# Kernel optimization log

Measured on AMD Instinct MI355X. Metric: run time of the kernel, lower is better.

Reference implementation:

```python
import jax, jax.numpy as jnp
import numpy as np

C = 1.0          # Poincare ball curvature
EPS = 1e-7       # clamp epsilon used by the torch code


def _expmap0(u, c=C):
    # geoopt PoincareBall.expmap0: tanh(sqrt(c)||u||) * u / (sqrt(c)||u||)
    sc = jnp.sqrt(c)
    n = jnp.maximum(jnp.linalg.norm(u, axis=-1, keepdims=True), 1e-15)
    return jnp.tanh(sc * n) * u / (sc * n)


def _hyp_dist_sq(x, y, c=C):
    # Pairwise squared Poincare distance WITHOUT materializing [nq,nc,d]:
    # d(x,y) = (2/sqrt(c)) * artanh(sqrt(c) * ||mobius_add(-x, y)||)
    # ||mobius_add(-x,y)||^2 expands into dot products and squared norms.
    dot = x @ y.T                                  # [nq, nc]
    xn = jnp.sum(x * x, axis=-1)[:, None]          # [nq, 1]
    yn = jnp.sum(y * y, axis=-1)[None, :]          # [1, nc]
    alpha = 1.0 - 2.0 * c * dot + c * yn
    beta = 1.0 - c * xn
    num_sq = alpha * alpha * xn - 2.0 * alpha * beta * dot + beta * beta * yn
    den = jnp.maximum(1.0 - 2.0 * c * dot + c * c * xn * yn, 1e-15)
    t = jnp.sqrt(c) * jnp.sqrt(jnp.maximum(num_sq, 0.0)) / den
    t = jnp.clip(t, 0.0, 1.0 - EPS)
    d = (2.0 / jnp.sqrt(c)) * jnp.arctanh(t)
    return d * d


def _project(x, We, be, Wh, bh, Ws, bs, scale_h):
    e = x @ We.T + be
    e = e / jnp.linalg.norm(e, axis=-1, keepdims=True)
    h = _expmap0((x @ Wh.T + bh) * scale_h)
    s = x @ Ws.T + bs
    s = s / jnp.linalg.norm(s, axis=-1, keepdims=True)
    return e, h, s


def setup_inputs() -> dict:
    key = jax.random.key(0)
    ks = jax.random.split(key, 12)
    D, NQ, NC = 768, 512, 65536
    def lin(k, out_d, in_d):
        lim = 1.0 / np.sqrt(in_d)
        k1, k2 = jax.random.split(k)
        W = jax.random.uniform(k1, (out_d, in_d), jnp.float32, -lim, lim)
        b = jax.random.uniform(k2, (out_d,), jnp.float32, -lim, lim)
        return W, b
    We, be = lin(ks[0], 32, D)
    Wh, bh = lin(ks[1], 16, D)
    Ws, bs = lin(ks[2], 16, D)
    W1, b1 = lin(ks[3], 32, D)
    W2, b2 = lin(ks[4], 3, 32)
    return {
        'x_q': jax.random.normal(ks[5], (NQ, D), jnp.float32),
        'x_c': jax.random.normal(ks[6], (NC, D), jnp.float32),
        'We': We, 'be': be, 'Wh': Wh, 'bh': bh, 'Ws': Ws, 'bs': bs,
        'scale_h': jnp.float32(0.3),
        'W1': W1, 'b1': b1, 'W2': W2, 'b2': b2,
    }


def reference(x_q, x_c, We, be, Wh, bh, Ws, bs, scale_h, W1, b1, W2, b2):
    # forward() projections for queries and corpus
    q_e, q_h, q_s = _project(x_q, We, be, Wh, bh, Ws, bs, scale_h)
    c_e, c_h, c_s = _project(x_c, We, be, Wh, bh, Ws, bs, scale_h)
    # get_weights(): softplus MLP on raw query embedding -> [nq, 3]
    w = jax.nn.softplus(jax.nn.relu(x_q @ W1.T + b1) @ W2.T + b2)
    # batch_retrieve math, fully vectorized
    dist_e = 2.0 - 2.0 * (q_e @ c_e.T)                       # unit vecs: ||a-b||^2
    dots = jnp.clip(q_s @ c_s.T, -1.0 + EPS, 1.0 - EPS)
    dist_s = jnp.arccos(dots) ** 2
    dist_h = _hyp_dist_sq(q_h, c_h)
    total = w[:, 0:1] * dist_e + w[:, 1:2] * dist_h + w[:, 2:3] * dist_s
    return -total
```

## Files before the change

kernel.cpp:

```cpp
#include <hip/hip_runtime.h>
#include <math.h>

#define NQ 512
#define NC 65536
#define DIM 768
#define PC_ROWS 128

typedef unsigned short u16;
typedef float f32x4 __attribute__((ext_vector_type(4)));
typedef short bf16x8 __attribute__((ext_vector_type(8)));

#define MFMA16(A, B, C) __builtin_amdgcn_mfma_f32_16x16x32_bf16(A, B, C, 0, 0, 0)

__device__ __forceinline__ u16 f2bf(float x) {
  union { float f; unsigned int u; } v; v.f = x;
  unsigned int r = v.u + 0x7fffu + ((v.u >> 16) & 1u);
  return (u16)(r >> 16);
}
__device__ __forceinline__ float bf2f(u16 h) {
  union { unsigned int u; float f; } v; v.u = ((unsigned int)h) << 16;
  return v.f;
}

__device__ __forceinline__ float acos_poly(float x) {
  float z = fabsf(x);
  float p = -0.0012624911f;
  p = fmaf(p, z, 0.0066700901f);
  p = fmaf(p, z, -0.0170881256f);
  p = fmaf(p, z, 0.0308918810f);
  p = fmaf(p, z, -0.0501743046f);
  p = fmaf(p, z, 0.0889789874f);
  p = fmaf(p, z, -0.2145988016f);
  p = fmaf(p, z, 1.5707963050f);
  float r = __builtin_amdgcn_sqrtf(1.0f - z) * p;
  return (x < 0.0f) ? (3.14159265358979f - r) : r;
}

__global__ __launch_bounds__(256) void transpose_w(
    const float* __restrict__ We, const float* __restrict__ Ws,
    const float* __restrict__ Wh, float* __restrict__ wt)
{
  int id = blockIdx.x * 256 + threadIdx.x;
  int k = id >> 6;
  int o = id & 63;
  float v = (o < 32) ? We[(size_t)o * DIM + k]
          : (o < 48) ? Ws[(size_t)(o - 32) * DIM + k]
                     : Wh[(size_t)(o - 48) * DIM + k];
  wt[id] = v;
}

__global__ __launch_bounds__(128) void proj_q(
    const float* __restrict__ xq,
    const float* __restrict__ We, const float* __restrict__ be,
    const float* __restrict__ Wh, const float* __restrict__ bh,
    const float* __restrict__ Ws, const float* __restrict__ bs,
    const float* __restrict__ shp,
    const float* __restrict__ W1, const float* __restrict__ b1,
    const float* __restrict__ W2, const float* __restrict__ b2,
    u16* __restrict__ qpak, float* __restrict__ qmeta)
{
  __shared__ __align__(16) float xrow[DIM];
  __shared__ float vals[96];
  __shared__ float reluv[32];
  __shared__ float hv[16];
  __shared__ float stats[8];
  const int t = threadIdx.x;
  const int q = blockIdx.x;

  for (int i = t; i < DIM; i += 128) xrow[i] = xq[(size_t)q * DIM + i];
  __syncthreads();

  if (t < 96) {
    const float* wr;
    float bias;
    if (t < 32)      { wr = We + (size_t)t * DIM;        bias = be[t]; }
    else if (t < 48) { wr = Ws + (size_t)(t - 32) * DIM; bias = bs[t - 32]; }
    else if (t < 64) { wr = Wh + (size_t)(t - 48) * DIM; bias = bh[t - 48]; }
    else             { wr = W1 + (size_t)(t - 64) * DIM; bias = b1[t - 64]; }
    const float4* x4 = (const float4*)xrow;
    const float4* w4 = (const float4*)wr;
    float acc = 0.0f;
    #pragma unroll 4
    for (int k = 0; k < DIM / 4; ++k) {
      float4 a = x4[k];
      float4 b = w4[k];
      acc = fmaf(a.x, b.x, acc);
      acc = fmaf(a.y, b.y, acc);
      acc = fmaf(a.z, b.z, acc);
      acc = fmaf(a.w, b.w, acc);
    }
    acc += bias;
    if (t >= 48 && t < 64) acc *= shp[0];
    vals[t] = acc;
  }
  __syncthreads();
  if (t < 32) reluv[t] = fmaxf(vals[64 + t], 0.0f);
  __syncthreads();

  if (t == 0) {
    float s = 0.0f;
    for (int j = 0; j < 32; ++j) s += vals[j] * vals[j];
    stats[0] = sqrtf(s);
  } else if (t == 1) {
    float s = 0.0f;
    for (int j = 32; j < 48; ++j) s += vals[j] * vals[j];
    stats[1] = sqrtf(s);
  } else if (t == 2) {
    float s = 0.0f;
    for (int j = 48; j < 64; ++j) s += vals[j] * vals[j];
    float n = fmaxf(sqrtf(s), 1e-15f);
    float f = tanhf(n) / n;
    float xn = 0.0f;
    for (int j = 0; j < 16; ++j) {
      float hj = vals[48 + j] * f;
      hv[j] = hj;
      xn += hj * hj;
    }
    stats[2] = xn;
    stats[3] = 1.0f - xn;
  } else if (t >= 3 && t < 6) {
    int m = t - 3;
    float s = 0.0f;
    for (int j = 0; j < 32; ++j) s = fmaf(reluv[j], W2[m * 32 + j], s);
    s += b2[m];
    stats[4 + m] = fmaxf(s, 0.0f) + log1pf(expf(-fabsf(s)));
  }
  __syncthreads();

  u16* qp = qpak + (size_t)q * 192;
  if (t < 32) {
    float v = vals[t] / stats[0];
    u16 hi = f2bf(v);
    u16 lo = f2bf(v - bf2f(hi));
    qp[t] = hi; qp[32 + t] = lo;
  } else if (t < 48) {
    int j = t - 32;
    float v = vals[t] / stats[1];
    u16 hi = f2bf(v);
    u16 lo = f2bf(v - bf2f(hi));
    qp[64 + j] = hi;  qp[80 + j] = hi;
    qp[96 + j] = lo;  qp[112 + j] = lo;
  } else if (t < 64) {
    int j = t - 48;
    float v = hv[j];
    u16 hi = f2bf(v);
    u16 lo = f2bf(v - bf2f(hi));
    qp[128 + j] = hi; qp[144 + j] = hi;
    qp[160 + j] = lo; qp[176 + j] = lo;
  } else if (t == 64) qmeta[(size_t)q * 8 + 0] = stats[2];
  else if (t == 65)   qmeta[(size_t)q * 8 + 1] = stats[3];
  else if (t >= 66 && t < 69) qmeta[(size_t)q * 8 + (t - 64)] = stats[4 + (t - 66)];
}

__global__ __launch_bounds__(512) void proj_corpus(
    const float* __restrict__ xc, const float* __restrict__ wt,
    const float* __restrict__ be, const float* __restrict__ bh,
    const float* __restrict__ bs, const float* __restrict__ shp,
    u16* __restrict__ cpak, float* __restrict__ cyn)
{
  __shared__ float lds[8320];
  float (*lxT)[132] = (float(*)[132])lds;
  float (*vals)[65] = (float(*)[65])lds;

  const int tid = threadIdx.x;
  const int lane = tid & 63;
  const int wv = __builtin_amdgcn_readfirstlane(tid >> 6);
  const int o0 = wv * 8;
  const int r0 = blockIdx.x * PC_ROWS;

  float acc0[8], acc1[8];
  #pragma unroll
  for (int j = 0; j < 8; ++j) { acc0[j] = 0.0f; acc1[j] = 0.0f; }

  for (int k0 = 0; k0 < DIM; k0 += 32) {
    __syncthreads();
    #pragma unroll
    for (int i = 0; i < 2; ++i) {
      int p = tid + 512 * i;
      int row = p >> 3;
      int kq = p & 7;
      const float4 v = *(const float4*)(xc + (size_t)(r0 + row) * DIM + k0 + 4 * kq);
      lxT[4 * kq + 0][row] = v.x;
      lxT[4 * kq + 1][row] = v.y;
      lxT[4 * kq + 2][row] = v.z;
      lxT[4 * kq + 3][row] = v.w;
    }
    __syncthreads();
    #pragma unroll
    for (int k = 0; k < 32; ++k) {
      const float xv0 = lxT[k][lane];
      const float xv1 = lxT[k][lane + 64];
      const float* wk = wt + (size_t)(k0 + k) * 64 + o0;
      #pragma unroll
      for (int j = 0; j < 8; ++j) {
        const float w = wk[j];
        acc0[j] = fmaf(xv0, w, acc0[j]);
        acc1[j] = fmaf(xv1, w, acc1[j]);
      }
    }
  }
  __syncthreads();

  const float sh = shp[0];
  #pragma unroll
  for (int j = 0; j < 8; ++j) {
    int o = o0 + j;
    float b = (o < 32) ? be[o] : (o < 48) ? bs[o - 32] : bh[o - 48];
    float v0 = acc0[j] + b;
    float v1 = acc1[j] + b;
    if (o >= 48) { v0 *= sh; v1 *= sh; }
    vals[lane][o] = v0;
    vals[lane + 64][o] = v1;
  }
  __syncthreads();

  const int part = tid >> 7;
  const int row = tid & 127;
  const size_t g = (size_t)(r0 + row);
  u16* cp = cpak + g * 128;
  if (part == 0) {
    float ssum = 0.0f;
    for (int j = 0; j < 32; ++j) ssum += vals[row][j] * vals[row][j];
    float inv = 1.0f / sqrtf(ssum);
    for (int j = 0; j < 32; ++j) {
      float v = vals[row][j] * inv;
      u16 hi = f2bf(v);
      cp[j] = hi;
      cp[32 + j] = f2bf(v - bf2f(hi));
    }
  } else if (part == 1) {
    float ssum = 0.0f;
    for (int j = 32; j < 48; ++j) ssum += vals[row][j] * vals[row][j];
    float inv = 1.0f / sqrtf(ssum);
    for (int j = 0; j < 16; ++j) {
      float v = vals[row][32 + j] * inv;
      u16 hi = f2bf(v);
      cp[64 + j] = hi;
      cp[80 + j] = f2bf(v - bf2f(hi));
    }
  } else if (part == 2) {
    float ssum = 0.0f;
    for (int j = 48; j < 64; ++j) ssum += vals[row][j] * vals[row][j];
    float n = fmaxf(sqrtf(ssum), 1e-15f);
    float f = tanhf(n) / n;
    float yn = 0.0f;
    for (int j = 0; j < 16; ++j) {
      float hj = vals[row][48 + j] * f;
      u16 hi = f2bf(hj);
      cp[96 + j] = hi;
      cp[112 + j] = f2bf(hj - bf2f(hi));
      yn += hj * hj;
    }
    cyn[g] = yn;
  }
}

#define CLIPC 0.99999988f

__device__ __forceinline__ float pair_score(
    float de, float dss, float dh,
    float xn, float beta, float w0, float w1, float w2, float yn)
{
  float dist_e = 2.0f - 2.0f * de;

  float dcl = fminf(fmaxf(dss, -CLIPC), CLIPC);
  float ac = acos_poly(dcl);
  float dist_s = ac * ac;

  float alpha = 1.0f - 2.0f * dh + yn;
  float ab = alpha * beta;
  float num = alpha * alpha * xn - 2.0f * ab * dh + beta * beta * yn;
  float den = fmaxf(1.0f - 2.0f * dh + xn * yn, 1e-15f);
  float t = __builtin_amdgcn_sqrtf(fmaxf(num, 0.0f)) * __builtin_amdgcn_rcpf(den);
  t = fminf(t, CLIPC);
  float dd = __logf((1.0f + t) * __builtin_amdgcn_rcpf(1.0f - t));
  float dist_h = dd * dd;

  return -(w0 * dist_e + w1 * dist_h + w2 * dist_s);
}

__global__ __launch_bounds__(256) void pairwise(
    const u16* __restrict__ cpak, const float* __restrict__ cyn,
    const u16* __restrict__ qpak, const float* __restrict__ qmeta,
    float* __restrict__ out)
{
  const int lane = threadIdx.x & 63;
  const int wv = threadIdx.x >> 6;
  const int lr = lane & 15;
  const int lg = lane >> 4;
  const int c0 = blockIdx.x * 128 + wv * 32;
  const int qbase = blockIdx.y * 256;

  bf16x8 Beh[2], Bel[2], Bsp[2], Bhp[2];
  float ynv[2];
  #pragma unroll
  for (int ct = 0; ct < 2; ++ct) {
    const u16* cb = cpak + (size_t)(c0 + ct * 16 + lr) * 128 + lg * 8;
    Beh[ct] = *(const bf16x8*)(cb + 0);
    Bel[ct] = *(const bf16x8*)(cb + 32);
    Bsp[ct] = *(const bf16x8*)(cb + 64);
    Bhp[ct] = *(const bf16x8*)(cb + 96);
    ynv[ct] = cyn[c0 + ct * 16 + lr];
  }

  #pragma unroll 1
  for (int qt = 0; qt < 16; ++qt) {
    const int q0 = qbase + qt * 16;
    const u16* qb = qpak + (size_t)(q0 + lr) * 192 + lg * 8;
    bf16x8 Aeh = *(const bf16x8*)(qb + 0);
    bf16x8 Ael = *(const bf16x8*)(qb + 32);
    bf16x8 Ash = *(const bf16x8*)(qb + 64);
    bf16x8 Asl = *(const bf16x8*)(qb + 96);
    bf16x8 Ahh = *(const bf16x8*)(qb + 128);
    bf16x8 Ahl = *(const bf16x8*)(qb + 160);

    float4 mv[4];
    float w2v[4];
    #pragma unroll
    for (int j = 0; j < 4; ++j) {
      const int q = q0 + lg * 4 + j;
      mv[j] = *(const float4*)(qmeta + (size_t)q * 8);
      w2v[j] = qmeta[(size_t)q * 8 + 4];
    }

    const f32x4 z = {0.0f, 0.0f, 0.0f, 0.0f};
    f32x4 aE[2], aS[2], aH[2];
    #pragma unroll
    for (int ct = 0; ct < 2; ++ct) {
      aE[ct] = MFMA16(Aeh, Beh[ct], z);
      aE[ct] = MFMA16(Ael, Beh[ct], aE[ct]);
      aE[ct] = MFMA16(Aeh, Bel[ct], aE[ct]);
      aS[ct] = MFMA16(Ash, Bsp[ct], z);
      aS[ct] = MFMA16(Asl, Bsp[ct], aS[ct]);
      aH[ct] = MFMA16(Ahh, Bhp[ct], z);
      aH[ct] = MFMA16(Ahl, Bhp[ct], aH[ct]);
    }

    #pragma unroll
    for (int j = 0; j < 4; ++j) {
      const int q = q0 + lg * 4 + j;
      #pragma unroll
      for (int ct = 0; ct < 2; ++ct) {
        float r = pair_score(aE[ct][j], aS[ct][j], aH[ct][j],
                             mv[j].x, mv[j].y, mv[j].z, mv[j].w, w2v[j],
                             ynv[ct]);
        out[(size_t)q * NC + c0 + ct * 16 + lr] = r;
      }
    }
  }
}

extern "C" void kernel_launch(void* const* d_in, const int* in_sizes, int n_in,
                              void* d_out, int out_size, void* d_ws, size_t ws_size,
                              hipStream_t stream) {
  const float* xq = (const float*)d_in[0];
  const float* xc = (const float*)d_in[1];
  const float* We = (const float*)d_in[2];
  const float* be = (const float*)d_in[3];
  const float* Wh = (const float*)d_in[4];
  const float* bh = (const float*)d_in[5];
  const float* Ws = (const float*)d_in[6];
  const float* bs = (const float*)d_in[7];
  const float* sh = (const float*)d_in[8];
  const float* W1 = (const float*)d_in[9];
  const float* b1 = (const float*)d_in[10];
  const float* W2 = (const float*)d_in[11];
  const float* b2 = (const float*)d_in[12];
  float* out = (float*)d_out;

  float* w = (float*)d_ws;
  u16* qpak = (u16*)w;
  float* qmeta = w + 49152;
  float* wt = qmeta + NQ * 8;
  u16* cpak = (u16*)(wt + DIM * 64);
  float* cyn = (wt + DIM * 64) + 4194304;

  transpose_w<<<DIM * 64 / 256, 256, 0, stream>>>(We, Ws, Wh, wt);
  proj_q<<<NQ, 128, 0, stream>>>(xq, We, be, Wh, bh, Ws, bs, sh, W1, b1, W2, b2,
                                 qpak, qmeta);
  proj_corpus<<<NC / PC_ROWS, 512, 0, stream>>>(xc, wt, be, bh, bs, sh, cpak, cyn);
  pairwise<<<dim3(NC / 128, 2, 1), 256, 0, stream>>>(cpak, cyn, qpak, qmeta, out);
}
```

Measured before the change: 476.0 us.

## Compute corpus projection with split-bf16 MFMA instead of scalar FMA

Replaces the scalar fp32 FMA loop in the corpus projection (65536x768 times 768x64) with bf16 MFMA 16x16x32. Each operand is split into hi and lo bf16 parts, and three products are accumulated to keep near-fp32 accuracy. Weights are pre-packed into the MFMA B-fragment layout by a new kernel. x tiles are converted to bf16 hi/lo and stored in LDS with an XOR swizzle. Block size drops to 256 threads, and the normalization epilogue is merged into two thread groups. The change targets the compute-bound FMA cost of the projection, which reads about 200 MB of x_c. It adds conversion work on the load path and slightly reduces precision.

```diff
diff --git a/kernel.cpp b/kernel.cpp
--- a/kernel.cpp
+++ b/kernel.cpp
@@ -20,6 +20,9 @@
 __device__ __forceinline__ float bf2f(u16 h) {
   union { unsigned int u; float f; } v; v.u = ((unsigned int)h) << 16;
   return v.f;
+}
+__device__ __forceinline__ unsigned int pk2(u16 a, u16 b) {
+  return (unsigned int)a | ((unsigned int)b << 16);
 }
 
 __device__ __forceinline__ float acos_poly(float x) {
@@ -36,17 +39,26 @@
   return (x < 0.0f) ? (3.14159265358979f - r) : r;
 }
 
-__global__ __launch_bounds__(256) void transpose_w(
+__global__ __launch_bounds__(256) void build_wpak(
     const float* __restrict__ We, const float* __restrict__ Ws,
-    const float* __restrict__ Wh, float* __restrict__ wt)
+    const float* __restrict__ Wh, u16* __restrict__ wpak)
 {
   int id = blockIdx.x * 256 + threadIdx.x;
-  int k = id >> 6;
-  int o = id & 63;
-  float v = (o < 32) ? We[(size_t)o * DIM + k]
-          : (o < 48) ? Ws[(size_t)(o - 32) * DIM + k]
-                     : Wh[(size_t)(o - 48) * DIM + k];
-  wt[id] = v;
+  int j = id & 7;
+  int lane = (id >> 3) & 63;
+  int nt = (id >> 9) & 3;
+  int kc = id >> 11;
+  int o = nt * 16 + (lane & 15);
+  int k = kc * 32 + ((lane >> 4) & 3) * 8 + j;
+  const float* Wrow = (o < 32) ? We + (size_t)o * DIM
+                    : (o < 48) ? Ws + (size_t)(o - 32) * DIM
+                               : Wh + (size_t)(o - 48) * DIM;
+  float w = Wrow[k];
+  u16 hi = f2bf(w);
+  u16 lo = f2bf(w - bf2f(hi));
+  size_t base = (((size_t)kc * 4 + nt) * 2 * 64 + lane) * 8 + j;
+  wpak[base] = hi;
+  wpak[base + 512] = lo;
 }
 
 __global__ __launch_bounds__(128) void proj_q(
@@ -149,69 +161,98 @@
     qp[160 + j] = lo; qp[176 + j] = lo;
   } else if (t == 64) qmeta[(size_t)q * 8 + 0] = stats[2];
   else if (t == 65)   qmeta[(size_t)q * 8 + 1] = stats[3];
-  else if (t >= 66 && t < 69) qmeta[(size_t)q * 8 + (t - 64)] = stats[4 + (t - 66)];
-}
-
-__global__ __launch_bounds__(512) void proj_corpus(
-    const float* __restrict__ xc, const float* __restrict__ wt,
+  else if (t >= 66 && t < 69) qmeta[(size_t)q * 8 + (t - 66 + 2)] = stats[4 + (t - 66)];
+}
+
+__global__ __launch_bounds__(256) void proj_corpus(
+    const float* __restrict__ xc, const u16* __restrict__ wpak,
     const float* __restrict__ be, const float* __restrict__ bh,
     const float* __restrict__ bs, const float* __restrict__ shp,
     u16* __restrict__ cpak, float* __restrict__ cyn)
 {
   __shared__ float lds[8320];
-  float (*lxT)[132] = (float(*)[132])lds;
+  u16* xpk = (u16*)lds;
   float (*vals)[65] = (float(*)[65])lds;
+  __shared__ float biasc[64];
+  __shared__ float shv;
 
   const int tid = threadIdx.x;
   const int lane = tid & 63;
-  const int wv = __builtin_amdgcn_readfirstlane(tid >> 6);
-  const int o0 = wv * 8;
+  const int wv = tid >> 6;
+  const int lr = lane & 15;
+  const int lg = lane >> 4;
   const int r0 = blockIdx.x * PC_ROWS;
 
-  float acc0[8], acc1[8];
+  if (tid < 64) {
+    biasc[tid] = (tid < 32) ? be[tid] : (tid < 48) ? bs[tid - 32] : bh[tid - 48];
+    if (tid == 0) shv = shp[0];
+  }
+
+  f32x4 acc[2][4];
   #pragma unroll
-  for (int j = 0; j < 8; ++j) { acc0[j] = 0.0f; acc1[j] = 0.0f; }
-
-  for (int k0 = 0; k0 < DIM; k0 += 32) {
+  for (int rt = 0; rt < 2; ++rt)
+    #pragma unroll
+    for (int nt = 0; nt < 4; ++nt)
+      acc[rt][nt] = (f32x4){0.0f, 0.0f, 0.0f, 0.0f};
+
+  for (int kc = 0; kc < 24; ++kc) {
     __syncthreads();
     #pragma unroll
-    for (int i = 0; i < 2; ++i) {
-      int p = tid + 512 * i;
+    for (int i = 0; i < 4; ++i) {
+      int p = tid + 256 * i;
       int row = p >> 3;
       int kq = p & 7;
-      const float4 v = *(const float4*)(xc + (size_t)(r0 + row) * DIM + k0 + 4 * kq);
-      lxT[4 * kq + 0][row] = v.x;
-      lxT[4 * kq + 1][row] = v.y;
-      lxT[4 * kq + 2][row] = v.z;
-      lxT[4 * kq + 3][row] = v.w;
+      const float4 v = *(const float4*)(xc + (size_t)(r0 + row) * DIM + kc * 32 + 4 * kq);
+      u16 hx = f2bf(v.x), hy = f2bf(v.y), hz = f2bf(v.z), hw = f2bf(v.w);
+      u16 lx = f2bf(v.x - bf2f(hx)), ly = f2bf(v.y - bf2f(hy));
+      u16 lz = f2bf(v.z - bf2f(hz)), lw = f2bf(v.w - bf2f(hw));
+      uint2 hvv = {pk2(hx, hy), pk2(hz, hw)};
+      uint2 lvv = {pk2(lx, ly), pk2(lz, lw)};
+      int rm = row & 7;
+      int qh = (kq >> 1) ^ rm;
+      int ql = (4 + (kq >> 1)) ^ rm;
+      int half = (kq & 1) * 8;
+      *(uint2*)((char*)xpk + row * 128 + qh * 16 + half) = hvv;
+      *(uint2*)((char*)xpk + row * 128 + ql * 16 + half) = lvv;
     }
     __syncthreads();
-    #pragma unroll
-    for (int k = 0; k < 32; ++k) {
-      const float xv0 = lxT[k][lane];
-      const float xv1 = lxT[k][lane + 64];
-      const float* wk = wt + (size_t)(k0 + k) * 64 + o0;
+
+    const u16* wb = wpak + (size_t)kc * 4096;
+    bf16x8 Bh[4], Bl[4];
+    #pragma unroll
+    for (int nt = 0; nt < 4; ++nt) {
+      Bh[nt] = *(const bf16x8*)(wb + (nt * 2 + 0) * 512 + lane * 8);
+      Bl[nt] = *(const bf16x8*)(wb + (nt * 2 + 1) * 512 + lane * 8);
+    }
+
+    #pragma unroll
+    for (int rt = 0; rt < 2; ++rt) {
+      int rowi = wv * 32 + rt * 16 + lr;
+      int rm = rowi & 7;
+      bf16x8 Ah = *(const bf16x8*)((const char*)xpk + rowi * 128 + (lg ^ rm) * 16);
+      bf16x8 Al = *(const bf16x8*)((const char*)xpk + rowi * 128 + ((4 + lg) ^ rm) * 16);
       #pragma unroll
-      for (int j = 0; j < 8; ++j) {
-        const float w = wk[j];
-        acc0[j] = fmaf(xv0, w, acc0[j]);
-        acc1[j] = fmaf(xv1, w, acc1[j]);
+      for (int nt = 0; nt < 4; ++nt) {
+        acc[rt][nt] = MFMA16(Ah, Bh[nt], acc[rt][nt]);
+        acc[rt][nt] = MFMA16(Al, Bh[nt], acc[rt][nt]);
+        acc[rt][nt] = MFMA16(Ah, Bl[nt], acc[rt][nt]);
       }
     }
   }
   __syncthreads();
 
-  const float sh = shp[0];
   #pragma unroll
-  for (int j = 0; j < 8; ++j) {
-    int o = o0 + j;
-    float b = (o < 32) ? be[o] : (o < 48) ? bs[o - 32] : bh[o - 48];
-    float v0 = acc0[j] + b;
-    float v1 = acc1[j] + b;
-    if (o >= 48) { v0 *= sh; v1 *= sh; }
-    vals[lane][o] = v0;
-    vals[lane + 64][o] = v1;
-  }
+  for (int rt = 0; rt < 2; ++rt)
+    #pragma unroll
+    for (int nt = 0; nt < 4; ++nt)
+      #pragma unroll
+      for (int reg = 0; reg < 4; ++reg) {
+        int row = wv * 32 + rt * 16 + lg * 4 + reg;
+        int o = nt * 16 + lr;
+        float v = acc[rt][nt][reg] + biasc[o];
+        if (o >= 48) v *= shv;
+        vals[row][o] = v;
+      }
   __syncthreads();
 
   const int part = tid >> 7;
@@ -228,7 +269,7 @@
       cp[j] = hi;
       cp[32 + j] = f2bf(v - bf2f(hi));
     }
-  } else if (part == 1) {
+  } else {
     float ssum = 0.0f;
     for (int j = 32; j < 48; ++j) ssum += vals[row][j] * vals[row][j];
     float inv = 1.0f / sqrtf(ssum);
@@ -238,10 +279,9 @@
       cp[64 + j] = hi;
       cp[80 + j] = f2bf(v - bf2f(hi));
     }
-  } else if (part == 2) {
-    float ssum = 0.0f;
-    for (int j = 48; j < 64; ++j) ssum += vals[row][j] * vals[row][j];
-    float n = fmaxf(sqrtf(ssum), 1e-15f);
+    float hsum = 0.0f;
+    for (int j = 48; j < 64; ++j) hsum += vals[row][j] * vals[row][j];
+    float n = fmaxf(sqrtf(hsum), 1e-15f);
     float f = tanhf(n) / n;
     float yn = 0.0f;
     for (int j = 0; j < 16; ++j) {
@@ -371,13 +411,14 @@
   float* w = (float*)d_ws;
   u16* qpak = (u16*)w;
   float* qmeta = w + 49152;
-  float* wt = qmeta + NQ * 8;
-  u16* cpak = (u16*)(wt + DIM * 64);
-  float* cyn = (wt + DIM * 64) + 4194304;
-
-  transpose_w<<<DIM * 64 / 256, 256, 0, stream>>>(We, Ws, Wh, wt);
+  u16* wpak = (u16*)(qmeta + NQ * 8);
+  float* base2 = qmeta + NQ * 8 + 49152;
+  u16* cpak = (u16*)base2;
+  float* cyn = base2 + 4194304;
+
+  build_wpak<<<192, 256, 0, stream>>>(We, Ws, Wh, wpak);
   proj_q<<<NQ, 128, 0, stream>>>(xq, We, be, Wh, bh, Ws, bs, sh, W1, b1, W2, b2,
                                  qpak, qmeta);
-  proj_corpus<<<NC / PC_ROWS, 512, 0, stream>>>(xc, wt, be, bh, bs, sh, cpak, cyn);
+  proj_corpus<<<NC / PC_ROWS, 256, 0, stream>>>(xc, wpak, be, bh, bs, sh, cpak, cyn);
   pairwise<<<dim3(NC / 128, 2, 1), 256, 0, stream>>>(cpak, cyn, qpak, qmeta, out);
 }
```

Result: faster. 445.6 us (-6.4%).
